# Kernel tuning notes

Measured on AMD Instinct MI355X. Metric: run time of the kernel, lower is better.

The kernel has to match this reference:

```python
import jax, jax.numpy as jnp
import numpy as np

B, N, D = 8, 2048, 128
AVG_DEG = 16.0        # expected out-degree of random binary adjacency
SEED_FRAC = 0.005     # fraction of initially-active nodes in state vector


def setup_inputs() -> dict:
    key = jax.random.key(0)
    ka, ks, kf = jax.random.split(key, 3)
    # Binary adjacency [B, N, N], avg degree ~16
    a = (jax.random.uniform(ka, (B, N, N)) < (AVG_DEG / N)).astype(jnp.float32)
    # Sparse binary seed state [B, N]; guarantee at least one seed per batch
    s = (jax.random.uniform(ks, (B, N)) < SEED_FRAC).astype(jnp.float32)
    s = s.at[:, 0].set(1.0)
    fea_emb = jax.random.normal(kf, (N, D), dtype=jnp.float32)
    return {
        "a": a,
        "s": s,
        "fea_emb": fea_emb,
        "alpha": jnp.float32(0.8),
        "step_num": 4,
    }


def reference(a, s, fea_emb, alpha, step_num):
    # fea = sum_n fea_emb[n] * s[b,n] * alpha   -> [B, D]
    fea = jnp.einsum('nd,bn->bd', fea_emb, s) * alpha

    def step(carry, i):
        s_cur, fea_cur = carry
        # 1-hop neighborhood reachability: batched adjacency matvec [B, N]
        neis = jnp.einsum('bio,bi->bo', a, s_cur)
        cover = ((s_cur > 0) | (neis > 0)).astype(s_cur.dtype)
        new_explore = cover - s_cur  # newly covered nodes this step
        # Original code skips the add when no new nodes; adding an all-zero
        # contribution is mathematically identical, so we add unconditionally.
        fea_cur = fea_cur + jnp.einsum('nd,bn->bd', fea_emb, new_explore) * alpha ** (i + 2)
        return (cover, fea_cur), None

    if step_num > 0:
        (cover, fea), _ = jax.lax.scan(step, (s, fea), jnp.arange(step_num, dtype=jnp.float32))
        denom = jnp.sum(cover, axis=-1, keepdims=True)  # [B, 1]
    else:
        denom = jnp.ones((s.shape[0], 1), dtype=s.dtype)  # cover = ones(B,1)
    return fea / denom
```

## Files before the change

kernel.cpp:

```cpp
#include <hip/hip_runtime.h>

#define BATCH 8
#define NN    2048
#define DD    128
#define STEPS 4
#define NCH   16
#define XGRID 1024
#define TPB   256


__global__ __launch_bounds__(TPB)
void init_kernel(const float* __restrict__ s, int* __restrict__ level,
                 int* __restrict__ cnt, int* __restrict__ flist0,
                 int* __restrict__ fcount0, float* __restrict__ out) {
    int b = blockIdx.x;
    __shared__ int sc;
    if (threadIdx.x == 0) sc = 0;
    __syncthreads();
    int local = 0;
    for (int n = threadIdx.x; n < NN; n += TPB) {
        float v = s[b * NN + n];
        int lv = (v > 0.0f) ? 0 : -1;
        level[b * NN + n] = lv;
        if (lv == 0) {
            local++;
            int idx = atomicAdd(fcount0, 1);
            flist0[idx] = (b << 16) | n;
        }
    }
    atomicAdd(&sc, local);
    for (int d = threadIdx.x; d < DD; d += TPB) out[b * DD + d] = 0.0f;
    __syncthreads();
    if (threadIdx.x == 0) atomicAdd(&cnt[b], sc);
}

__global__ __launch_bounds__(TPB)
void expand_kernel(const float* __restrict__ a, int* __restrict__ level,
                   int* __restrict__ cnt,
                   const int* __restrict__ flin, const int* __restrict__ fcin,
                   int* __restrict__ flout, int* __restrict__ fcout, int t) {
    __shared__ int lbuf[NN];
    __shared__ int lcnt, lbase;
    int fc = *fcin;
    for (int e = blockIdx.x; e < fc; e += XGRID) {
        int pair = flin[e];
        int b = pair >> 16, i = pair & 0xffff;
        int* lv = level + b * NN;
        if (threadIdx.x == 0) lcnt = 0;
        __syncthreads();
        const int4* row = (const int4*)(a + (size_t)(b * NN + i) * NN);
        for (int c = threadIdx.x; c < NN / 4; c += TPB) {
            int4 v = row[c];
            if ((v.x | v.y | v.z | v.w) == 0) continue;
            int o = c * 4;
            if (v.x && lv[o    ] < 0 && atomicCAS(&lv[o    ], -1, t) == -1) lbuf[atomicAdd(&lcnt, 1)] = o;
            if (v.y && lv[o + 1] < 0 && atomicCAS(&lv[o + 1], -1, t) == -1) lbuf[atomicAdd(&lcnt, 1)] = o + 1;
            if (v.z && lv[o + 2] < 0 && atomicCAS(&lv[o + 2], -1, t) == -1) lbuf[atomicAdd(&lcnt, 1)] = o + 2;
            if (v.w && lv[o + 3] < 0 && atomicCAS(&lv[o + 3], -1, t) == -1) lbuf[atomicAdd(&lcnt, 1)] = o + 3;
        }
        __syncthreads();
        if (threadIdx.x == 0 && lcnt > 0) {
            lbase = atomicAdd(fcout, lcnt);
            atomicAdd(&cnt[b], lcnt);
        }
        __syncthreads();
        int nfound = lcnt;
        for (int k = threadIdx.x; k < nfound; k += TPB)
            flout[lbase + k] = (b << 16) | lbuf[k];
        __syncthreads();
    }
}

__global__ __launch_bounds__(DD)
void finalize_kernel(const float* __restrict__ fea_emb,
                     const int* __restrict__ level,
                     const int* __restrict__ cnt,
                     const float* __restrict__ alpha_p,
                     float* __restrict__ out) {
    int b  = blockIdx.x / NCH;
    int ch = blockIdx.x % NCH;
    int n0 = ch * (NN / NCH);
    __shared__ float w[NN / NCH];
    float alpha = *alpha_p;
    float pw[STEPS + 1];
    pw[0] = alpha;
#pragma unroll
    for (int k = 1; k <= STEPS; k++) pw[k] = pw[k - 1] * alpha;

    int tid = threadIdx.x;
    int l = level[b * NN + n0 + tid];
    w[tid] = (l >= 0) ? pw[l] : 0.0f;
    __syncthreads();

    float acc = 0.0f;
#pragma unroll 4
    for (int r = 0; r < NN / NCH; r++) {
        float wr = w[r];
        if (wr != 0.0f) acc += wr * fea_emb[(size_t)(n0 + r) * DD + tid];
    }
    float invD = 1.0f / (float)cnt[b];
    atomicAdd(&out[b * DD + tid], acc * invD);
}

extern "C" void kernel_launch(void* const* d_in, const int* in_sizes, int n_in,
                              void* d_out, int out_size, void* d_ws, size_t ws_size,
                              hipStream_t stream) {
    const float* a       = (const float*)d_in[0];
    const float* s       = (const float*)d_in[1];
    const float* fea_emb = (const float*)d_in[2];
    const float* alpha   = (const float*)d_in[3];
    float* out = (float*)d_out;

    char* ws    = (char*)d_ws;
    int* level  = (int*)ws;
    int* cnt    = (int*)(ws + 65536);
    int* fcount = (int*)(ws + 65536 + 64);
    int* flist  = (int*)(ws + 131072);

    hipMemsetAsync(ws + 65536, 0, 128, stream);

    init_kernel<<<BATCH, TPB, 0, stream>>>(s, level, cnt, flist, fcount, out);
    for (int t = 1; t <= STEPS; t++)
        expand_kernel<<<XGRID, TPB, 0, stream>>>(
            a, level, cnt,
            flist + (size_t)(t - 1) * BATCH * NN, fcount + (t - 1),
            flist + (size_t)t * BATCH * NN,       fcount + t, t);
    finalize_kernel<<<BATCH * NCH, DD, 0, stream>>>(fea_emb, level, cnt, alpha, out);
}
```

Baseline: 333.4 us.

## Fuse init, BFS expansion steps, and finalize into one persistent kernel with grid barriers

Merges the six separate launches (init, four frontier-expansion steps, finalize) into a single persistent kernel of 1024 blocks that synchronizes phases with a software grid barrier built on an atomic counter and spin-wait. It is meant to remove per-launch overhead and the inter-kernel gaps that dominate this small sparse BFS workload. The finalize stage is reshaped to 256 threads per block, with each half handling 64 rows and reading the level array directly. The risk is that the barrier relies on all 1024 blocks being co-resident, and its spin loop has a bailout that could silently break synchronization.

New measurement: 1.113 ms. +233.7%, slower.

```diff
diff --git a/kernel.cpp b/kernel.cpp
--- a/kernel.cpp
+++ b/kernel.cpp
@@ -4,102 +4,100 @@
 #define NN    2048
 #define DD    128
 #define STEPS 4
-#define NCH   16
-#define XGRID 1024
+#define GRID  1024
 #define TPB   256
 
 
-__global__ __launch_bounds__(TPB)
-void init_kernel(const float* __restrict__ s, int* __restrict__ level,
-                 int* __restrict__ cnt, int* __restrict__ flist0,
-                 int* __restrict__ fcount0, float* __restrict__ out) {
-    int b = blockIdx.x;
-    __shared__ int sc;
-    if (threadIdx.x == 0) sc = 0;
+__device__ __forceinline__ void grid_barrier(int* bar, int target) {
     __syncthreads();
-    int local = 0;
-    for (int n = threadIdx.x; n < NN; n += TPB) {
-        float v = s[b * NN + n];
-        int lv = (v > 0.0f) ? 0 : -1;
-        level[b * NN + n] = lv;
-        if (lv == 0) {
-            local++;
-            int idx = atomicAdd(fcount0, 1);
-            flist0[idx] = (b << 16) | n;
+    if (threadIdx.x == 0) {
+        __threadfence();
+        __hip_atomic_fetch_add(bar, 1, __ATOMIC_ACQ_REL, __HIP_MEMORY_SCOPE_AGENT);
+        int spins = 0;
+        while (__hip_atomic_load(bar, __ATOMIC_ACQUIRE, __HIP_MEMORY_SCOPE_AGENT) < target) {
+            __builtin_amdgcn_s_sleep(8);
+            if (++spins > (1 << 22)) break;
         }
+        __threadfence();
     }
-    atomicAdd(&sc, local);
-    for (int d = threadIdx.x; d < DD; d += TPB) out[b * DD + d] = 0.0f;
     __syncthreads();
-    if (threadIdx.x == 0) atomicAdd(&cnt[b], sc);
 }
 
 __global__ __launch_bounds__(TPB)
-void expand_kernel(const float* __restrict__ a, int* __restrict__ level,
-                   int* __restrict__ cnt,
-                   const int* __restrict__ flin, const int* __restrict__ fcin,
-                   int* __restrict__ flout, int* __restrict__ fcout, int t) {
+void fused_kernel(const float* __restrict__ a, const float* __restrict__ s,
+                  const float* __restrict__ fea_emb, const float* __restrict__ alpha_p,
+                  float* __restrict__ out,
+                  int* __restrict__ level, int* __restrict__ cnt,
+                  int* __restrict__ fcount, int* __restrict__ bar,
+                  int* __restrict__ flist) {
+    const int bid = blockIdx.x, tid = threadIdx.x;
+    const int gid = bid * TPB + tid;
+
+    if (gid < BATCH * NN) {
+        int b = gid >> 11, n = gid & (NN - 1);
+        int lv = (s[gid] > 0.0f) ? 0 : -1;
+        level[gid] = lv;
+        if (lv == 0) {
+            int idx = atomicAdd(&fcount[0], 1);
+            flist[idx] = (b << 16) | n;
+            atomicAdd(&cnt[b], 1);
+        }
+    }
+    if (gid < BATCH * DD) out[gid] = 0.0f;
+    grid_barrier(bar, GRID * 1);
+
     __shared__ int lbuf[NN];
     __shared__ int lcnt, lbase;
-    int fc = *fcin;
-    for (int e = blockIdx.x; e < fc; e += XGRID) {
-        int pair = flin[e];
-        int b = pair >> 16, i = pair & 0xffff;
-        int* lv = level + b * NN;
-        if (threadIdx.x == 0) lcnt = 0;
-        __syncthreads();
-        const int4* row = (const int4*)(a + (size_t)(b * NN + i) * NN);
-        for (int c = threadIdx.x; c < NN / 4; c += TPB) {
-            int4 v = row[c];
-            if ((v.x | v.y | v.z | v.w) == 0) continue;
-            int o = c * 4;
-            if (v.x && lv[o    ] < 0 && atomicCAS(&lv[o    ], -1, t) == -1) lbuf[atomicAdd(&lcnt, 1)] = o;
-            if (v.y && lv[o + 1] < 0 && atomicCAS(&lv[o + 1], -1, t) == -1) lbuf[atomicAdd(&lcnt, 1)] = o + 1;
-            if (v.z && lv[o + 2] < 0 && atomicCAS(&lv[o + 2], -1, t) == -1) lbuf[atomicAdd(&lcnt, 1)] = o + 2;
-            if (v.w && lv[o + 3] < 0 && atomicCAS(&lv[o + 3], -1, t) == -1) lbuf[atomicAdd(&lcnt, 1)] = o + 3;
+    for (int t = 1; t <= STEPS; t++) {
+        int fc = fcount[t - 1];
+        const int* flin  = flist + (size_t)(t - 1) * BATCH * NN;
+        int*       flout = flist + (size_t)t * BATCH * NN;
+        for (int e = bid; e < fc; e += GRID) {
+            int pair = flin[e];
+            int b = pair >> 16, i = pair & 0xffff;
+            int* lv = level + b * NN;
+            if (tid == 0) lcnt = 0;
+            __syncthreads();
+            const int4* row = (const int4*)(a + (size_t)(b * NN + i) * NN);
+            for (int c = tid; c < NN / 4; c += TPB) {
+                int4 v = row[c];
+                if ((v.x | v.y | v.z | v.w) == 0) continue;
+                int o = c * 4;
+                if (v.x && lv[o    ] < 0 && atomicCAS(&lv[o    ], -1, t) == -1) lbuf[atomicAdd(&lcnt, 1)] = o;
+                if (v.y && lv[o + 1] < 0 && atomicCAS(&lv[o + 1], -1, t) == -1) lbuf[atomicAdd(&lcnt, 1)] = o + 1;
+                if (v.z && lv[o + 2] < 0 && atomicCAS(&lv[o + 2], -1, t) == -1) lbuf[atomicAdd(&lcnt, 1)] = o + 2;
+                if (v.w && lv[o + 3] < 0 && atomicCAS(&lv[o + 3], -1, t) == -1) lbuf[atomicAdd(&lcnt, 1)] = o + 3;
+            }
+            __syncthreads();
+            if (tid == 0 && lcnt > 0) {
+                lbase = atomicAdd(&fcount[t], lcnt);
+                atomicAdd(&cnt[b], lcnt);
+            }
+            __syncthreads();
+            for (int k = tid; k < lcnt; k += TPB)
+                flout[lbase + k] = (b << 16) | lbuf[k];
+            __syncthreads();
         }
-        __syncthreads();
-        if (threadIdx.x == 0 && lcnt > 0) {
-            lbase = atomicAdd(fcout, lcnt);
-            atomicAdd(&cnt[b], lcnt);
-        }
-        __syncthreads();
-        int nfound = lcnt;
-        for (int k = threadIdx.x; k < nfound; k += TPB)
-            flout[lbase + k] = (b << 16) | lbuf[k];
-        __syncthreads();
+        grid_barrier(bar, GRID * (1 + t));
     }
-}
 
-__global__ __launch_bounds__(DD)
-void finalize_kernel(const float* __restrict__ fea_emb,
-                     const int* __restrict__ level,
-                     const int* __restrict__ cnt,
-                     const float* __restrict__ alpha_p,
-                     float* __restrict__ out) {
-    int b  = blockIdx.x / NCH;
-    int ch = blockIdx.x % NCH;
-    int n0 = ch * (NN / NCH);
-    __shared__ float w[NN / NCH];
+    if (bid >= BATCH * 16) return;
+    int b = bid >> 4, ch = bid & 15;
+    int d = tid & (DD - 1), half = tid >> 7;
     float alpha = *alpha_p;
     float pw[STEPS + 1];
     pw[0] = alpha;
 #pragma unroll
     for (int k = 1; k <= STEPS; k++) pw[k] = pw[k - 1] * alpha;
-
-    int tid = threadIdx.x;
-    int l = level[b * NN + n0 + tid];
-    w[tid] = (l >= 0) ? pw[l] : 0.0f;
-    __syncthreads();
-
+    int r0 = ch * 128 + half * 64;
     float acc = 0.0f;
 #pragma unroll 4
-    for (int r = 0; r < NN / NCH; r++) {
-        float wr = w[r];
-        if (wr != 0.0f) acc += wr * fea_emb[(size_t)(n0 + r) * DD + tid];
+    for (int r = r0; r < r0 + 64; r++) {
+        int l = level[b * NN + r];
+        if (l >= 0) acc += pw[l] * fea_emb[(size_t)r * DD + d];
     }
     float invD = 1.0f / (float)cnt[b];
-    atomicAdd(&out[b * DD + tid], acc * invD);
+    atomicAdd(&out[b * DD + d], acc * invD);
 }
 
 extern "C" void kernel_launch(void* const* d_in, const int* in_sizes, int n_in,
@@ -114,16 +112,11 @@
     char* ws    = (char*)d_ws;
     int* level  = (int*)ws;
     int* cnt    = (int*)(ws + 65536);
-    int* fcount = (int*)(ws + 65536 + 64);
+    int* fcount = (int*)(ws + 65568);
+    int* bar    = (int*)(ws + 65600);
     int* flist  = (int*)(ws + 131072);
 
     hipMemsetAsync(ws + 65536, 0, 128, stream);
-
-    init_kernel<<<BATCH, TPB, 0, stream>>>(s, level, cnt, flist, fcount, out);
-    for (int t = 1; t <= STEPS; t++)
-        expand_kernel<<<XGRID, TPB, 0, stream>>>(
-            a, level, cnt,
-            flist + (size_t)(t - 1) * BATCH * NN, fcount + (t - 1),
-            flist + (size_t)t * BATCH * NN,       fcount + t, t);
-    finalize_kernel<<<BATCH * NCH, DD, 0, stream>>>(fea_emb, level, cnt, alpha, out);
+    fused_kernel<<<GRID, TPB, 0, stream>>>(a, s, fea_emb, alpha, out,
+                                           level, cnt, fcount, bar, flist);
 }
```
